# Performance work log

Hardware: AMD Instinct MI355X
Metric: run time of the kernel (lower is better)

## Reference

```python
import jax, jax.numpy as jnp
import numpy as np
import math

SEQLEN, DIM, N_HEADS = 2048, 4096, 32
HEAD_DIM = DIM // N_HEADS
NEG_INF = -1e30  # exp underflows to exactly 0, same effect as -inf without NaN risk


def setup_inputs() -> dict:
    key = jax.random.key(0)
    ks = jax.random.split(key, 7)
    scale = 1.0 / math.sqrt(DIM)
    x = jax.random.normal(ks[0], (SEQLEN, DIM), dtype=jnp.float32)
    weight_q = jax.random.normal(ks[1], (DIM, DIM), dtype=jnp.float32) * scale
    weight_k = jax.random.normal(ks[2], (DIM, DIM), dtype=jnp.float32) * scale
    weight_v = jax.random.normal(ks[3], (DIM, DIM), dtype=jnp.float32) * scale
    weight_o = jax.random.normal(ks[4], (DIM, DIM), dtype=jnp.float32) * scale
    # RoPE frequencies: freqs_cis = exp(i * t * theta_j), standard LLaMA schedule
    inv_freq = 1.0 / (10000.0 ** (np.arange(0, HEAD_DIM, 2, dtype=np.float32) / HEAD_DIM))
    angles = np.arange(SEQLEN, dtype=np.float32)[:, None] * inv_freq[None, :]  # [S, hd/2]
    freqs_cos = jnp.asarray(np.cos(angles), dtype=jnp.float32)
    freqs_sin = jnp.asarray(np.sin(angles), dtype=jnp.float32)
    # additive causal mask [S, S]
    mask = jnp.where(jnp.triu(jnp.ones((SEQLEN, SEQLEN), dtype=bool), k=1), NEG_INF, 0.0).astype(jnp.float32)
    return {"x": x, "weight_q": weight_q, "weight_k": weight_k, "weight_v": weight_v,
            "weight_o": weight_o, "freqs_cos": freqs_cos, "freqs_sin": freqs_sin,
            "mask": mask, "start_pos": 0}


def _apply_rope(t, cos, sin):
    # t: [S, H, hd]; cos/sin: [S, hd/2]
    tr = t.reshape(*t.shape[:-1], -1, 2)           # [S, H, hd/2, 2]
    t_re, t_im = tr[..., 0], tr[..., 1]
    c = cos[:, None, :]
    s = sin[:, None, :]
    out_re = t_re * c - t_im * s
    out_im = t_re * s + t_im * c
    return jnp.stack([out_re, out_im], axis=-1).reshape(t.shape)


def reference(x, weight_q, weight_k, weight_v, weight_o, freqs_cos, freqs_sin, mask, start_pos):
    S, D = x.shape
    hd = freqs_cos.shape[-1] * 2
    H = D // hd
    # the per-head double loop over wq[j][i] is exactly a full [D,D] projection
    xq = (x @ weight_q).reshape(S, H, hd)
    xk = (x @ weight_k).reshape(S, H, hd)
    xv = (x @ weight_v).reshape(S, H, hd)
    xq = _apply_rope(xq, freqs_cos, freqs_sin)
    xk = _apply_rope(xk, freqs_cos, freqs_sin)
    # start_pos == 0 prefill: cache slice == freshly computed keys/values
    scores = jnp.einsum('shd,thd->hst', xq, xk) / jnp.sqrt(jnp.float32(hd))
    scores = scores + mask[None, :, :]
    probs = jax.nn.softmax(scores.astype(jnp.float32), axis=-1).astype(xq.dtype)
    qkv = jnp.einsum('hst,thd->shd', probs, xv).reshape(S, D)
    return qkv @ weight_o
```

## Files before the change

kernel.cpp:

```cpp
#include <hip/hip_runtime.h>
#include <hip/hip_bf16.h>
#include <type_traits>

typedef __hip_bfloat16 bf16;
typedef __attribute__((ext_vector_type(8))) short s8v;
typedef __attribute__((ext_vector_type(4))) short s4v;
typedef __attribute__((ext_vector_type(4))) float f4v;

#define MFMA16(A, B, C) __builtin_amdgcn_mfma_f32_16x16x32_bf16((A), (B), (C), 0, 0, 0)

constexpr int SEQ = 2048;
constexpr int DIM = 4096;
constexpr int NH  = 32;
constexpr int HD  = 128;

__device__ __forceinline__ short f2bs(float f) {
    __hip_bfloat16_raw r = __float2bfloat16(f);
    return (short)r.x;
}

__device__ __forceinline__ void ld_g2l(const bf16* g, bf16* l) {
    __builtin_amdgcn_global_load_lds(
        (const __attribute__((address_space(1))) void*)g,
        (__attribute__((address_space(3))) void*)l, 16, 0, 0);
}

__global__ void convert_bf16(const float* __restrict__ s, bf16* __restrict__ d) {
    int i = blockIdx.x * blockDim.x + threadIdx.x;
    float4 f = ((const float4*)s)[i];
    s4v o;
    o[0] = f2bs(f.x); o[1] = f2bs(f.y); o[2] = f2bs(f.z); o[3] = f2bs(f.w);
    *(s4v*)(d + (size_t)i * 4) = o;
}

__global__ void convt_bf16(const float* __restrict__ src, bf16* __restrict__ dst,
                           int R, int C) {
    __shared__ float t[32][33];
    int c0 = blockIdx.x * 32, r0 = blockIdx.y * 32;
    int tx = threadIdx.x, ty = threadIdx.y;
#pragma unroll
    for (int i = 0; i < 4; i++)
        t[ty + 8 * i][tx] = src[(size_t)(r0 + ty + 8 * i) * C + c0 + tx];
    __syncthreads();
#pragma unroll
    for (int i = 0; i < 4; i++)
        dst[(size_t)(c0 + ty + 8 * i) * R + r0 + tx] = __float2bfloat16(t[tx][ty + 8 * i]);
}

template <typename CT>
__global__ __launch_bounds__(512, 2) void gemm_8p(const bf16* __restrict__ A,
                                                  const bf16* __restrict__ Bt,
                                                  CT* __restrict__ C,
                                                  int M, int N, int K) {
    __shared__ bf16 As_[2][128 * 64];
    __shared__ bf16 Bs_[2][256 * 64];
    const int tid  = threadIdx.x;
    const int lane = tid & 63;
    const int wv   = tid >> 6;
    const int m16  = lane & 15;
    const int quad = lane >> 4;
    const int wm   = wv >> 2, wn = wv & 3;
    const int bm   = blockIdx.y, bn = blockIdx.x;

    const bf16* Ab = A  + (size_t)bm * 128 * K;
    const bf16* Bb = Bt + (size_t)bn * 256 * K;

    const int i0   = wv * 64 + lane;
    const int row0 = i0 >> 3;
    const int gc8  = ((i0 & 7) ^ (row0 & 7)) * 8;
    const int dst0 = (wv * 64) * 8;
    const int dst1 = (512 + wv * 64) * 8;

    const int aB = (wm * 64 + m16) * 64;
    const int bB = (wn * 64 + m16) * 64;
    const int swz = m16 & 7;
    const int c0k = ((0 + quad) ^ swz) * 8;
    const int c1k = ((4 + quad) ^ swz) * 8;

    const int NT = K >> 6;

    f4v acc[4][4] = {};
    s8v aR[4][2], bR[4][2];

#define STAGEU(gb, lb) do { \
        ld_g2l((gb) + (size_t)row0 * K + gc8, (lb) + dst0); \
        ld_g2l((gb) + (size_t)(row0 + 64) * K + gc8, (lb) + dst1); } while (0)
#define LDA_(i, ks) aR[i][ks] = *(const s8v*)(Ac + aB + (i) * 1024 + ((ks) ? c1k : c0k))
#define LDB_(j, ks) bR[j][ks] = *(const s8v*)(Bc + bB + (j) * 1024 + ((ks) ? c1k : c0k))
#define MMQ(i, j) do { acc[i][j] = MFMA16(aR[i][0], bR[j][0], acc[i][j]); \
                       acc[i][j] = MFMA16(aR[i][1], bR[j][1], acc[i][j]); } while (0)
#define BARX()  __builtin_amdgcn_s_barrier()
#define LGKM0() do { asm volatile("s_waitcnt lgkmcnt(0)" ::: "memory"); \
                     __builtin_amdgcn_sched_barrier(0); } while (0)

    STAGEU(Ab, As_[0]);
    STAGEU(Bb, Bs_[0]);
    STAGEU(Bb + (size_t)128 * K, Bs_[0] + 128 * 64);
    if (NT > 1) {
        STAGEU(Bb + 64, Bs_[1]);
        STAGEU(Bb + (size_t)128 * K + 64, Bs_[1] + 128 * 64);
        STAGEU(Ab + 64, As_[1]);
        asm volatile("s_waitcnt vmcnt(6)" ::: "memory");
    } else {
        asm volatile("s_waitcnt vmcnt(0)" ::: "memory");
    }
    __builtin_amdgcn_sched_barrier(0);
    BARX();

    for (int t = 0; t < NT; ++t) {
        const int cur = t & 1;
        const bf16* Ac = As_[cur];
        const bf16* Bc = Bs_[cur];
        const bool more = (t + 2 < NT);
        const int k2 = (t + 2) << 6;

        LDA_(0, 0); LDA_(0, 1); LDA_(1, 0); LDA_(1, 1);
        LDB_(0, 0); LDB_(0, 1); LDB_(1, 0); LDB_(1, 1);
        BARX(); LGKM0();
        __builtin_amdgcn_s_setprio(1);
        MMQ(0, 0); MMQ(0, 1); MMQ(1, 0); MMQ(1, 1);
        __builtin_amdgcn_s_setprio(0);
        BARX();

        LDB_(2, 0); LDB_(2, 1); LDB_(3, 0); LDB_(3, 1);
        BARX(); LGKM0();
        __builtin_amdgcn_s_setprio(1);
        MMQ(0, 2); MMQ(0, 3); MMQ(1, 2); MMQ(1, 3);
        __builtin_amdgcn_s_setprio(0);
        BARX();

        LDA_(2, 0); LDA_(2, 1); LDA_(3, 0); LDA_(3, 1);
        if (more) {
            STAGEU(Bb + k2, Bs_[cur]);
            STAGEU(Bb + (size_t)128 * K + k2, Bs_[cur] + 128 * 64);
        }
        BARX(); LGKM0();
        __builtin_amdgcn_s_setprio(1);
        MMQ(2, 0); MMQ(2, 1); MMQ(3, 0); MMQ(3, 1);
        __builtin_amdgcn_s_setprio(0);
        BARX();

        if (more) {
            STAGEU(Ab + k2, As_[cur]);
            asm volatile("s_waitcnt vmcnt(6)" ::: "memory");
        } else {
            asm volatile("s_waitcnt vmcnt(0)" ::: "memory");
        }
        __builtin_amdgcn_sched_barrier(0);
        BARX();
        __builtin_amdgcn_s_setprio(1);
        MMQ(2, 2); MMQ(2, 3); MMQ(3, 2); MMQ(3, 3);
        __builtin_amdgcn_s_setprio(0);
        BARX();
    }

#undef STAGEU
#undef LDA_
#undef LDB_
#undef MMQ
#undef BARX
#undef LGKM0

#pragma unroll
    for (int i = 0; i < 4; i++)
#pragma unroll
        for (int j = 0; j < 4; j++)
#pragma unroll
            for (int r = 0; r < 4; r++) {
                int row = bm * 128 + wm * 64 + i * 16 + quad * 4 + r;
                int col = bn * 256 + wn * 64 + j * 16 + m16;
                if constexpr (std::is_same<CT, float>::value)
                    C[(size_t)row * N + col] = acc[i][j][r];
                else
                    C[(size_t)row * N + col] = __float2bfloat16(acc[i][j][r]);
            }
}

template <typename AT, typename CT>
__global__ __launch_bounds__(256) void gemm_nat(const AT* __restrict__ A,
                                                const float* __restrict__ B,
                                                CT* __restrict__ C,
                                                int M, int N, int K) {
    __shared__ short As[128][40];
    __shared__ short Bs[128][40];
    const int tid  = threadIdx.x;
    const int lane = tid & 63;
    const int w    = tid >> 6;
    const int m16  = lane & 15;
    const int quad = lane >> 4;
    const int wm   = w >> 1, wn = w & 1;
    const int bm   = blockIdx.y, bn = blockIdx.x;

    const AT* Ab = A + (size_t)bm * 128 * K;

    f4v acc[4][4] = {};
    const int r0 = tid >> 2;
    const int kc = (tid & 3) * 8;

    for (int k0 = 0; k0 < K; k0 += 32) {
        if constexpr (std::is_same<AT, float>::value) {
#pragma unroll
            for (int half = 0; half < 2; half++) {
                const float* src = Ab + (size_t)(r0 + 64 * half) * K + k0 + kc;
                float4 f0 = *(const float4*)(src);
                float4 f1 = *(const float4*)(src + 4);
                s8v t;
                t[0] = f2bs(f0.x); t[1] = f2bs(f0.y); t[2] = f2bs(f0.z); t[3] = f2bs(f0.w);
                t[4] = f2bs(f1.x); t[5] = f2bs(f1.y); t[6] = f2bs(f1.z); t[7] = f2bs(f1.w);
                *(s8v*)&As[r0 + 64 * half][kc] = t;
            }
        } else {
            *(s8v*)&As[r0][kc]      = *(const s8v*)(Ab + (size_t)r0 * K + k0 + kc);
            *(s8v*)&As[r0 + 64][kc] = *(const s8v*)(Ab + (size_t)(r0 + 64) * K + k0 + kc);
        }
#pragma unroll
        for (int v = tid; v < 512; v += 256) {
            int kr = v >> 4;
            int nc = (v & 15) * 8;
            const float* src = B + (size_t)(k0 + kr) * N + bn * 128 + nc;
            float4 f0 = *(const float4*)(src);
            float4 f1 = *(const float4*)(src + 4);
            Bs[nc + 0][kr] = f2bs(f0.x); Bs[nc + 1][kr] = f2bs(f0.y);
            Bs[nc + 2][kr] = f2bs(f0.z); Bs[nc + 3][kr] = f2bs(f0.w);
            Bs[nc + 4][kr] = f2bs(f1.x); Bs[nc + 5][kr] = f2bs(f1.y);
            Bs[nc + 6][kr] = f2bs(f1.z); Bs[nc + 7][kr] = f2bs(f1.w);
        }
        __syncthreads();

        s8v a[4], b[4];
#pragma unroll
        for (int i = 0; i < 4; i++) a[i] = *(s8v*)&As[wm * 64 + i * 16 + m16][quad * 8];
#pragma unroll
        for (int j = 0; j < 4; j++) b[j] = *(s8v*)&Bs[wn * 64 + j * 16 + m16][quad * 8];
#pragma unroll
        for (int i = 0; i < 4; i++)
#pragma unroll
            for (int j = 0; j < 4; j++) acc[i][j] = MFMA16(a[i], b[j], acc[i][j]);
        __syncthreads();
    }

#pragma unroll
    for (int i = 0; i < 4; i++)
#pragma unroll
        for (int j = 0; j < 4; j++)
#pragma unroll
            for (int r = 0; r < 4; r++) {
                int row = bm * 128 + wm * 64 + i * 16 + quad * 4 + r;
                int col = bn * 128 + wn * 64 + j * 16 + m16;
                if constexpr (std::is_same<CT, float>::value)
                    C[(size_t)row * N + col] = acc[i][j][r];
                else
                    C[(size_t)row * N + col] = __float2bfloat16(acc[i][j][r]);
            }
}

__global__ void rope_kernel(bf16* __restrict__ Q, bf16* __restrict__ K,
                            const float* __restrict__ fc, const float* __restrict__ fs) {
    int tid = blockIdx.x * blockDim.x + threadIdx.x;
    int s = tid >> 11;
    int r = tid & 2047;
    int i = r & 63;
    float c  = fc[s * 64 + i];
    float sn = fs[s * 64 + i];
    size_t idx = (size_t)s * DIM + 2 * r;
    float qre = __bfloat162float(Q[idx]), qim = __bfloat162float(Q[idx + 1]);
    Q[idx]     = __float2bfloat16(qre * c - qim * sn);
    Q[idx + 1] = __float2bfloat16(qre * sn + qim * c);
    float kre = __bfloat162float(K[idx]), kim = __bfloat162float(K[idx + 1]);
    K[idx]     = __float2bfloat16(kre * c - kim * sn);
    K[idx + 1] = __float2bfloat16(kre * sn + kim * c);
}

__global__ __launch_bounds__(256) void attn_kernel(const bf16* __restrict__ Q,
                                                   const bf16* __restrict__ K,
                                                   const bf16* __restrict__ V,
                                                   bf16* __restrict__ O) {
    __shared__ short Ks[64][136];
    __shared__ short Vs[128][72];
    __shared__ short Ps[64][72];

    const int qb = (int)gridDim.x - 1 - (int)blockIdx.x;
    const int h  = blockIdx.y;
    const int tid  = threadIdx.x;
    const int w    = tid >> 6;
    const int lane = tid & 63;
    const int m16  = lane & 15;
    const int quad = lane >> 4;
    const float scale = 0.08838834764831845f;

    const int rn  = tid >> 4;
    const int rc  = (tid & 15) * 8;
    const int dcs = (tid & 15) & 7;

    s8v aq[4];
    {
        const bf16* qp = Q + (size_t)(qb * 64 + w * 16 + m16) * DIM + h * HD + quad * 8;
#pragma unroll
        for (int ks = 0; ks < 4; ks++) aq[ks] = *(const s8v*)(qp + ks * 32);
    }

    f4v acc[8] = {};
    float mrow[4] = {-1e30f, -1e30f, -1e30f, -1e30f};
    float lrow[4] = {};

    s8v kreg[4], vreg[4];
    {
        const bf16* kp = K + (size_t)rn * DIM + h * HD + rc;
        const bf16* vp = V + (size_t)rn * DIM + h * HD + rc;
#pragma unroll
        for (int it = 0; it < 4; it++) {
            kreg[it] = *(const s8v*)(kp + (size_t)it * 16 * DIM);
            vreg[it] = *(const s8v*)(vp + (size_t)it * 16 * DIM);
        }
    }

    for (int kt = 0; kt <= qb; kt++) {
#pragma unroll
        for (int it = 0; it < 4; it++)
            *(s8v*)&Ks[it * 16 + rn][rc] = kreg[it];
#pragma unroll
        for (int it = 0; it < 4; it++) {
            int n   = it * 16 + rn;
            int col = (((n >> 3) ^ dcs) << 3) | (n & 7);
#pragma unroll
            for (int e = 0; e < 8; e++) Vs[rc + e][col] = vreg[it][e];
        }
        __syncthreads();

        if (kt < qb) {
            const bf16* kp = K + (size_t)((kt + 1) * 64 + rn) * DIM + h * HD + rc;
            const bf16* vp = V + (size_t)((kt + 1) * 64 + rn) * DIM + h * HD + rc;
#pragma unroll
            for (int it = 0; it < 4; it++) {
                kreg[it] = *(const s8v*)(kp + (size_t)it * 16 * DIM);
                vreg[it] = *(const s8v*)(vp + (size_t)it * 16 * DIM);
            }
        }

        f4v sc[4] = {};
#pragma unroll
        for (int j = 0; j < 4; j++)
#pragma unroll
            for (int ks = 0; ks < 4; ks++) {
                s8v bk = *(s8v*)&Ks[j * 16 + m16][ks * 32 + quad * 8];
                sc[j] = MFMA16(aq[ks], bk, sc[j]);
            }

        const bool diag = (kt == qb);
#pragma unroll
        for (int j = 0; j < 4; j++)
#pragma unroll
            for (int r = 0; r < 4; r++) {
                float sv = sc[j][r] * scale;
                if (diag && (j * 16 + m16) > (w * 16 + quad * 4 + r)) sv = -1e30f;
                sc[j][r] = sv;
            }

#pragma unroll
        for (int r = 0; r < 4; r++) {
            float mx = fmaxf(fmaxf(sc[0][r], sc[1][r]), fmaxf(sc[2][r], sc[3][r]));
#pragma unroll
            for (int off = 1; off < 16; off <<= 1) mx = fmaxf(mx, __shfl_xor(mx, off, 64));
            float mn    = fmaxf(mrow[r], mx);
            float alpha = __expf(mrow[r] - mn);
            mrow[r] = mn;
            float rs = 0.f;
#pragma unroll
            for (int j = 0; j < 4; j++) {
                float p = __expf(sc[j][r] - mn);
                sc[j][r] = p;
                rs += p;
            }
#pragma unroll
            for (int off = 1; off < 16; off <<= 1) rs += __shfl_xor(rs, off, 64);
            lrow[r] = lrow[r] * alpha + rs;
#pragma unroll
            for (int jo = 0; jo < 8; jo++) acc[jo][r] = acc[jo][r] * alpha;
        }

#pragma unroll
        for (int j = 0; j < 4; j++)
#pragma unroll
            for (int r = 0; r < 4; r++)
                Ps[w * 16 + quad * 4 + r][j * 16 + m16] = f2bs(sc[j][r]);
        asm volatile("s_waitcnt lgkmcnt(0)" ::: "memory");
        __builtin_amdgcn_sched_barrier(0);

#pragma unroll
        for (int ks2 = 0; ks2 < 2; ks2++) {
            s8v ap = *(s8v*)&Ps[w * 16 + m16][ks2 * 32 + quad * 8];
#pragma unroll
            for (int jo = 0; jo < 8; jo++) {
                int dv = jo * 16 + m16;
                int cg = (((ks2 * 4 + quad) ^ ((dv >> 3) & 7)) << 3);
                s8v bv = *(s8v*)&Vs[dv][cg];
                acc[jo] = MFMA16(ap, bv, acc[jo]);
            }
        }
        __syncthreads();
    }

#pragma unroll
    for (int jo = 0; jo < 8; jo++)
#pragma unroll
        for (int r = 0; r < 4; r++) {
            float o = acc[jo][r] / fmaxf(lrow[r], 1e-30f);
            int row = qb * 64 + w * 16 + quad * 4 + r;
            int col = h * HD + jo * 16 + m16;
            O[(size_t)row * DIM + col] = __float2bfloat16(o);
        }
}

extern "C" void kernel_launch(void* const* d_in, const int* in_sizes, int n_in,
                              void* d_out, int out_size, void* d_ws, size_t ws_size,
                              hipStream_t stream) {
    const float* x  = (const float*)d_in[0];
    const float* wq = (const float*)d_in[1];
    const float* wk = (const float*)d_in[2];
    const float* wv = (const float*)d_in[3];
    const float* wo = (const float*)d_in[4];
    const float* fc = (const float*)d_in[5];
    const float* fs = (const float*)d_in[6];

    float* out = (float*)d_out;

    const size_t SZ = (size_t)SEQ * DIM;
    const size_t WZ = (size_t)DIM * DIM;
    bf16* Q  = (bf16*)d_ws;
    bf16* Kb = Q + SZ;
    bf16* V  = Kb + SZ;
    bf16* AO = V + SZ;

    const size_t need = (5 * SZ + WZ) * sizeof(bf16);

    if (ws_size >= need) {
        bf16* xb = AO + SZ;
        bf16* wb = xb + SZ;

        dim3 tB(32, 8), tGw(DIM / 32, DIM / 32);
        dim3 gG8(DIM / 256, SEQ / 128);

        convert_bf16<<<(int)(SZ / 4 / 256), 256, 0, stream>>>(x, xb);

        convt_bf16<<<tGw, tB, 0, stream>>>(wq, wb, DIM, DIM);
        gemm_8p<bf16><<<gG8, 512, 0, stream>>>(xb, wb, Q, SEQ, DIM, DIM);
        convt_bf16<<<tGw, tB, 0, stream>>>(wk, wb, DIM, DIM);
        gemm_8p<bf16><<<gG8, 512, 0, stream>>>(xb, wb, Kb, SEQ, DIM, DIM);
        convt_bf16<<<tGw, tB, 0, stream>>>(wv, wb, DIM, DIM);
        gemm_8p<bf16><<<gG8, 512, 0, stream>>>(xb, wb, V, SEQ, DIM, DIM);

        rope_kernel<<<(SEQ * (DIM / 2)) / 256, 256, 0, stream>>>(Q, Kb, fc, fs);
        attn_kernel<<<dim3(SEQ / 64, NH), 256, 0, stream>>>(Q, Kb, V, AO);

        convt_bf16<<<tGw, tB, 0, stream>>>(wo, wb, DIM, DIM);
        gemm_8p<float><<<gG8, 512, 0, stream>>>(AO, wb, out, SEQ, DIM, DIM);
    } else {
        dim3 gGn(DIM / 128, SEQ / 128);
        gemm_nat<float, bf16><<<gGn, 256, 0, stream>>>(x, wq, Q,  SEQ, DIM, DIM);
        gemm_nat<float, bf16><<<gGn, 256, 0, stream>>>(x, wk, Kb, SEQ, DIM, DIM);
        gemm_nat<float, bf16><<<gGn, 256, 0, stream>>>(x, wv, V,  SEQ, DIM, DIM);
        rope_kernel<<<(SEQ * (DIM / 2)) / 256, 256, 0, stream>>>(Q, Kb, fc, fs);
        attn_kernel<<<dim3(SEQ / 64, NH), 256, 0, stream>>>(Q, Kb, V, AO);
        gemm_nat<bf16, float><<<gGn, 256, 0, stream>>>(AO, wo, out, SEQ, DIM, DIM);
    }
}
```

Before: 836.8 us.

## Triple-buffer GEMM LDS stages with one barrier per k-step and vectorize weight transpose

The bf16 GEMM moves from double- to triple-buffered LDS. Each k-step now issues the global-to-LDS prefetch for tile t+2 into a free buffer up front, loads all A/B fragments, runs all 16 MFMA pairs, and synchronizes with a single barrier instead of many. This aims to cut barrier stalls and let loads overlap compute better, at the cost of about 144KB of LDS per block. The fp32-to-bf16 weight transpose kernel is also rewritten to use 64x64 tiles with float4 reads and 16-byte bf16 writes, which reduces memory transactions.

```diff
diff --git a/kernel.cpp b/kernel.cpp
--- a/kernel.cpp
+++ b/kernel.cpp
@@ -33,27 +33,41 @@
     *(s4v*)(d + (size_t)i * 4) = o;
 }
 
-__global__ void convt_bf16(const float* __restrict__ src, bf16* __restrict__ dst,
-                           int R, int C) {
-    __shared__ float t[32][33];
-    int c0 = blockIdx.x * 32, r0 = blockIdx.y * 32;
-    int tx = threadIdx.x, ty = threadIdx.y;
-#pragma unroll
-    for (int i = 0; i < 4; i++)
-        t[ty + 8 * i][tx] = src[(size_t)(r0 + ty + 8 * i) * C + c0 + tx];
+__global__ __launch_bounds__(256) void convt_bf16(const float* __restrict__ src,
+                                                  bf16* __restrict__ dst,
+                                                  int R, int C) {
+    __shared__ float t[64][65];
+    const int c0 = blockIdx.x * 64, r0 = blockIdx.y * 64;
+    const int tid = threadIdx.x;
+    const int lr = tid >> 4;
+    const int lc = (tid & 15) * 4;
+#pragma unroll
+    for (int i = 0; i < 4; i++) {
+        float4 f = *(const float4*)(src + (size_t)(r0 + lr + 16 * i) * C + c0 + lc);
+        t[lr + 16 * i][lc]     = f.x;
+        t[lr + 16 * i][lc + 1] = f.y;
+        t[lr + 16 * i][lc + 2] = f.z;
+        t[lr + 16 * i][lc + 3] = f.w;
+    }
     __syncthreads();
-#pragma unroll
-    for (int i = 0; i < 4; i++)
-        dst[(size_t)(c0 + ty + 8 * i) * R + r0 + tx] = __float2bfloat16(t[tx][ty + 8 * i]);
+    const int oc = tid >> 2;
+#pragma unroll
+    for (int i = 0; i < 2; i++) {
+        int rr = (tid & 3) * 8 + 32 * i;
+        s8v o;
+#pragma unroll
+        for (int e = 0; e < 8; e++) o[e] = f2bs(t[rr + e][oc]);
+        *(s8v*)(dst + (size_t)(c0 + oc) * R + r0 + rr) = o;
+    }
 }
 
 template <typename CT>
-__global__ __launch_bounds__(512, 2) void gemm_8p(const bf16* __restrict__ A,
+__global__ __launch_bounds__(512, 2) void gemm_3b(const bf16* __restrict__ A,
                                                   const bf16* __restrict__ Bt,
                                                   CT* __restrict__ C,
                                                   int M, int N, int K) {
-    __shared__ bf16 As_[2][128 * 64];
-    __shared__ bf16 Bs_[2][256 * 64];
+    __shared__ bf16 As_[3][128 * 64];
+    __shared__ bf16 Bs_[3][256 * 64];
     const int tid  = threadIdx.x;
     const int lane = tid & 63;
     const int wv   = tid >> 6;
@@ -89,7 +103,6 @@
 #define LDB_(j, ks) bR[j][ks] = *(const s8v*)(Bc + bB + (j) * 1024 + ((ks) ? c1k : c0k))
 #define MMQ(i, j) do { acc[i][j] = MFMA16(aR[i][0], bR[j][0], acc[i][j]); \
                        acc[i][j] = MFMA16(aR[i][1], bR[j][1], acc[i][j]); } while (0)
-#define BARX()  __builtin_amdgcn_s_barrier()
 #define LGKM0() do { asm volatile("s_waitcnt lgkmcnt(0)" ::: "memory"); \
                      __builtin_amdgcn_sched_barrier(0); } while (0)
 
@@ -97,68 +110,57 @@
     STAGEU(Bb, Bs_[0]);
     STAGEU(Bb + (size_t)128 * K, Bs_[0] + 128 * 64);
     if (NT > 1) {
+        STAGEU(Ab + 64, As_[1]);
         STAGEU(Bb + 64, Bs_[1]);
         STAGEU(Bb + (size_t)128 * K + 64, Bs_[1] + 128 * 64);
-        STAGEU(Ab + 64, As_[1]);
         asm volatile("s_waitcnt vmcnt(6)" ::: "memory");
     } else {
         asm volatile("s_waitcnt vmcnt(0)" ::: "memory");
     }
     __builtin_amdgcn_sched_barrier(0);
-    BARX();
-
+    __builtin_amdgcn_s_barrier();
+
+    int cur = 0, nx2 = 2;
     for (int t = 0; t < NT; ++t) {
-        const int cur = t & 1;
         const bf16* Ac = As_[cur];
         const bf16* Bc = Bs_[cur];
         const bool more = (t + 2 < NT);
-        const int k2 = (t + 2) << 6;
+
+        if (more) {
+            const int k2 = (t + 2) << 6;
+            bf16* Ad = As_[nx2];
+            bf16* Bd = Bs_[nx2];
+            STAGEU(Ab + k2, Ad);
+            STAGEU(Bb + k2, Bd);
+            STAGEU(Bb + (size_t)128 * K + k2, Bd + 128 * 64);
+        }
 
         LDA_(0, 0); LDA_(0, 1); LDA_(1, 0); LDA_(1, 1);
+        LDA_(2, 0); LDA_(2, 1); LDA_(3, 0); LDA_(3, 1);
         LDB_(0, 0); LDB_(0, 1); LDB_(1, 0); LDB_(1, 1);
-        BARX(); LGKM0();
+        LDB_(2, 0); LDB_(2, 1); LDB_(3, 0); LDB_(3, 1);
+        LGKM0();
+
         __builtin_amdgcn_s_setprio(1);
-        MMQ(0, 0); MMQ(0, 1); MMQ(1, 0); MMQ(1, 1);
+        MMQ(0, 0); MMQ(0, 1); MMQ(0, 2); MMQ(0, 3);
+        MMQ(1, 0); MMQ(1, 1); MMQ(1, 2); MMQ(1, 3);
+        MMQ(2, 0); MMQ(2, 1); MMQ(2, 2); MMQ(2, 3);
+        MMQ(3, 0); MMQ(3, 1); MMQ(3, 2); MMQ(3, 3);
         __builtin_amdgcn_s_setprio(0);
-        BARX();
-
-        LDB_(2, 0); LDB_(2, 1); LDB_(3, 0); LDB_(3, 1);
-        BARX(); LGKM0();
-        __builtin_amdgcn_s_setprio(1);
-        MMQ(0, 2); MMQ(0, 3); MMQ(1, 2); MMQ(1, 3);
-        __builtin_amdgcn_s_setprio(0);
-        BARX();
-
-        LDA_(2, 0); LDA_(2, 1); LDA_(3, 0); LDA_(3, 1);
-        if (more) {
-            STAGEU(Bb + k2, Bs_[cur]);
-            STAGEU(Bb + (size_t)128 * K + k2, Bs_[cur] + 128 * 64);
-        }
-        BARX(); LGKM0();
-        __builtin_amdgcn_s_setprio(1);
-        MMQ(2, 0); MMQ(2, 1); MMQ(3, 0); MMQ(3, 1);
-        __builtin_amdgcn_s_setprio(0);
-        BARX();
-
-        if (more) {
-            STAGEU(Ab + k2, As_[cur]);
-            asm volatile("s_waitcnt vmcnt(6)" ::: "memory");
-        } else {
-            asm volatile("s_waitcnt vmcnt(0)" ::: "memory");
-        }
+
+        if (more) asm volatile("s_waitcnt vmcnt(6)" ::: "memory");
+        else      asm volatile("s_waitcnt vmcnt(0)" ::: "memory");
         __builtin_amdgcn_sched_barrier(0);
-        BARX();
-        __builtin_amdgcn_s_setprio(1);
-        MMQ(2, 2); MMQ(2, 3); MMQ(3, 2); MMQ(3, 3);
-        __builtin_amdgcn_s_setprio(0);
-        BARX();
+        __builtin_amdgcn_s_barrier();
+
+        cur = (cur == 2) ? 0 : cur + 1;
+        nx2 = (nx2 == 2) ? 0 : nx2 + 1;
     }
 
 #undef STAGEU
 #undef LDA_
 #undef LDB_
 #undef MMQ
-#undef BARX
 #undef LGKM0
 
 #pragma unroll
@@ -437,23 +439,23 @@
         bf16* xb = AO + SZ;
         bf16* wb = xb + SZ;
 
-        dim3 tB(32, 8), tGw(DIM / 32, DIM / 32);
+        dim3 tGw(DIM / 64, DIM / 64);
         dim3 gG8(DIM / 256, SEQ / 128);
 
         convert_bf16<<<(int)(SZ / 4 / 256), 256, 0, stream>>>(x, xb);
 
-        convt_bf16<<<tGw, tB, 0, stream>>>(wq, wb, DIM, DIM);
-        gemm_8p<bf16><<<gG8, 512, 0, stream>>>(xb, wb, Q, SEQ, DIM, DIM);
-        convt_bf16<<<tGw, tB, 0, stream>>>(wk, wb, DIM, DIM);
-        gemm_8p<bf16><<<gG8, 512, 0, stream>>>(xb, wb, Kb, SEQ, DIM, DIM);
-        convt_bf16<<<tGw, tB, 0, stream>>>(wv, wb, DIM, DIM);
-        gemm_8p<bf16><<<gG8, 512, 0, stream>>>(xb, wb, V, SEQ, DIM, DIM);
+        convt_bf16<<<tGw, 256, 0, stream>>>(wq, wb, DIM, DIM);
+        gemm_3b<bf16><<<gG8, 512, 0, stream>>>(xb, wb, Q, SEQ, DIM, DIM);
+        convt_bf16<<<tGw, 256, 0, stream>>>(wk, wb, DIM, DIM);
+        gemm_3b<bf16><<<gG8, 512, 0, stream>>>(xb, wb, Kb, SEQ, DIM, DIM);
+        convt_bf16<<<tGw, 256, 0, stream>>>(wv, wb, DIM, DIM);
+        gemm_3b<bf16><<<gG8, 512, 0, stream>>>(xb, wb, V, SEQ, DIM, DIM);
 
         rope_kernel<<<(SEQ * (DIM / 2)) / 256, 256, 0, stream>>>(Q, Kb, fc, fs);
         attn_kernel<<<dim3(SEQ / 64, NH), 256, 0, stream>>>(Q, Kb, V, AO);
 
-        convt_bf16<<<tGw, tB, 0, stream>>>(wo, wb, DIM, DIM);
-        gemm_8p<float><<<gG8, 512, 0, stream>>>(AO, wb, out, SEQ, DIM, DIM);
+        convt_bf16<<<tGw, 256, 0, stream>>>(wo, wb, DIM, DIM);
+        gemm_3b<float><<<gG8, 512, 0, stream>>>(AO, wb, out, SEQ, DIM, DIM);
     } else {
         dim3 gGn(DIM / 128, SEQ / 128);
         gemm_nat<float, bf16><<<gGn, 256, 0, stream>>>(x, wq, Q,  SEQ, DIM, DIM);
```

New measurement: 863.5 us. 3.2% more time.
